# Kernel tuning notes

Hardware: AMD Instinct MI355X
Metric: run time of the kernel (lower is better)

Reference implementation:

```python
import jax, jax.numpy as jnp
import numpy as np

NUM_BEAMS = 2


def setup_inputs() -> dict:
    key = jax.random.key(0)
    ks = jax.random.split(key, 5)
    B, T, H, E, F = 128, 32, 768, 4, 3072
    x = jax.random.normal(ks[0], (B, T, H), dtype=jnp.float32)
    Wg = jax.random.normal(ks[1], (E, H), dtype=jnp.float32) * (1.0 / np.sqrt(H))
    W1 = jax.random.normal(ks[2], (E, H, F), dtype=jnp.float32) * (1.0 / np.sqrt(H))
    b1 = jnp.zeros((E, F), dtype=jnp.float32)
    W2 = jax.random.normal(ks[3], (E, F, H), dtype=jnp.float32) * (1.0 / np.sqrt(F))
    b2 = jnp.zeros((E, H), dtype=jnp.float32)
    return {"x": x, "Wg": Wg, "W1": W1, "b1": b1, "W2": W2, "b2": b2}


def reference(x, Wg, W1, b1, W2, b2):
    B, T, H = x.shape
    E = Wg.shape[0]
    nb = NUM_BEAMS
    # ---- forward_gate: mask is all-ones, so masked mean == mean over tokens ----
    x_avg = jnp.mean(x, axis=1)                          # [B, H]
    logits_gate = x_avg @ Wg.T                           # [B, E]
    prob_gate = jax.nn.softmax(logits_gate, axis=-1)     # [B, E]
    # ---- importance auxiliary loss (torch.std uses ddof=1) ----
    importance = jnp.sum(prob_gate, axis=0)              # [E]
    importance_loss = (jnp.std(importance, ddof=1) / jnp.mean(importance)) ** 2
    # ---- beam search, first layer: exp(log(p)) == p, top-k per row ----
    current_scores = jnp.exp(jnp.log(prob_gate))         # == prob_gate (kept for fidelity)
    topk_values, gate_idx = jax.lax.top_k(current_scores, nb)   # [B, nb]
    beam_scores = topk_values.reshape(nb * B)            # row-major flatten, matches .view
    expert_route = gate_idx.reshape(nb * B)[:, None]     # [B*nb, 1]
    beam_idx = jnp.arange(nb * B)
    current_expert_select = expert_route[:, -1]          # [B*nb]
    # ---- first layer: replicate x and scores along beam dim (interleaved) ----
    x_rep = jnp.repeat(x, nb, axis=0)                    # [B*nb, T, H]
    scores_rep = jnp.repeat(prob_gate, nb, axis=0)       # [B*nb, E]
    # input_x = x_rep[beam_idx] is identity here (beam_idx == arange)
    # ---- forward_expert_ffn: run ALL experts, mask+combine with gate prob ----
    h1 = jnp.einsum('bth,ehf->betf', x_rep, W1) + b1[None, :, None, :]
    h1 = jax.nn.gelu(h1, approximate=False)              # torch GELU is exact erf form
    cand = jnp.einsum('betf,efh->beth', h1, W2) + b2[None, :, None, :]  # [B*nb, E, T, H]
    weight = scores_rep * jax.nn.one_hot(current_expert_select, E, dtype=scores_rep.dtype)
    output = jnp.einsum('beth,be->bth', cand, weight)    # weighted sum over experts
    return output, beam_scores, expert_route, beam_idx, importance_loss
```

## Files before the change

### kernel.cpp

```cpp
#include <hip/hip_runtime.h>
#include <math.h>

typedef _Float16 f16;
typedef _Float16 f16x8 __attribute__((ext_vector_type(8)));
typedef float f32x4 __attribute__((ext_vector_type(4)));

#define Bn 128
#define Tn 32
#define Hn 768
#define En 4
#define Fn 3072
#define Rn 256
#define MAXT 67

static constexpr size_t OUT_ELEMS  = (size_t)Rn*Tn*Hn;
static constexpr size_t SCORES_OFF = OUT_ELEMS;
static constexpr size_t ROUTE_OFF  = OUT_ELEMS + Rn;
static constexpr size_t BIDX_OFF   = OUT_ELEMS + 2*Rn;
static constexpr size_t LOSS_OFF   = OUT_ELEMS + 3*Rn;

#define WS_WSF    0u
#define WS_ROUTE  4096u
#define WS_GRP    8192u
#define WS_X16    16384u
#define WS_W1T    (WS_X16 + 2u*Bn*Tn*Hn)
#define WS_W2T    (WS_W1T + 2u*En*Hn*Fn)
#define WS_H1     (WS_W2T + 2u*En*Fn*Hn)

#define GLOAD16(g, l) __builtin_amdgcn_global_load_lds( \
    (const __attribute__((address_space(1))) unsigned int*)(g), \
    (__attribute__((address_space(3))) unsigned int*)(l), 16, 0, 0)

__device__ __forceinline__ float fast_gelu(float v) {
  float s = v * 0.70710678118f;
  float a = fabsf(s);
  float t = 1.0f / (1.0f + 0.3275911f * a);
  float y = t*(0.254829592f + t*(-0.284496736f + t*(1.421413741f +
            t*(-1.453152027f + t*1.061405429f))));
  float er = 1.0f - y * __expf(-a*a);
  er = (s < 0.0f) ? -er : er;
  return 0.5f * v * (1.0f + er);
}

__global__ __launch_bounds__(64) void gate_kernel(
    const float* __restrict__ x, const float* __restrict__ Wg,
    float* __restrict__ out, float* __restrict__ wsf, int* __restrict__ route)
{
  const int b = blockIdx.x;
  const int l = threadIdx.x;
  float acc0=0.f, acc1=0.f, acc2=0.f, acc3=0.f;
  const float* xb = x + (size_t)b*Tn*Hn;
  for (int h = l; h < Hn; h += 64) {
    float xa = 0.f;
    #pragma unroll
    for (int t = 0; t < Tn; ++t) xa += xb[t*Hn + h];
    xa *= (1.0f/Tn);
    acc0 += xa * Wg[0*Hn + h];
    acc1 += xa * Wg[1*Hn + h];
    acc2 += xa * Wg[2*Hn + h];
    acc3 += xa * Wg[3*Hn + h];
  }
  #pragma unroll
  for (int o = 32; o > 0; o >>= 1) {
    acc0 += __shfl_down(acc0, o);
    acc1 += __shfl_down(acc1, o);
    acc2 += __shfl_down(acc2, o);
    acc3 += __shfl_down(acc3, o);
  }
  if (l == 0) {
    float lg[4] = {acc0, acc1, acc2, acc3};
    float m = fmaxf(fmaxf(lg[0],lg[1]), fmaxf(lg[2],lg[3]));
    float p[4]; float s = 0.f;
    #pragma unroll
    for (int e = 0; e < 4; ++e) { p[e] = expf(lg[e]-m); s += p[e]; }
    float inv = 1.f/s;
    #pragma unroll
    for (int e = 0; e < 4; ++e) { p[e] *= inv; wsf[b*4+e] = p[e]; }
    int i1 = 0;
    #pragma unroll
    for (int e = 1; e < 4; ++e) if (p[e] > p[i1]) i1 = e;
    int i2 = (i1 == 0) ? 1 : 0;
    #pragma unroll
    for (int e = 0; e < 4; ++e) if (e != i1 && p[e] > p[i2]) i2 = e;
    int idx[2] = {i1, i2};
    #pragma unroll
    for (int k = 0; k < 2; ++k) {
      int r = 2*b + k;
      float pv = p[idx[k]];
      wsf[512 + r] = pv;
      route[r] = idx[k];
      out[SCORES_OFF + r] = pv;
      out[ROUTE_OFF  + r] = (float)idx[k];
      out[BIDX_OFF   + r] = (float)r;
    }
  }
}

__global__ __launch_bounds__(64) void loss_kernel(
    const float* __restrict__ wsf, float* __restrict__ out)
{
  const int l = threadIdx.x;
  float i0=0.f,i1=0.f,i2=0.f,i3=0.f;
  for (int b = l; b < Bn; b += 64) {
    i0 += wsf[b*4+0]; i1 += wsf[b*4+1]; i2 += wsf[b*4+2]; i3 += wsf[b*4+3];
  }
  #pragma unroll
  for (int o = 32; o > 0; o >>= 1) {
    i0 += __shfl_down(i0,o); i1 += __shfl_down(i1,o);
    i2 += __shfl_down(i2,o); i3 += __shfl_down(i3,o);
  }
  if (l == 0) {
    float mean = 0.25f*(i0+i1+i2+i3);
    float d0=i0-mean, d1=i1-mean, d2=i2-mean, d3=i3-mean;
    float var = (d0*d0+d1*d1+d2*d2+d3*d3) * (1.f/3.f);
    out[LOSS_OFF] = var / (mean*mean);
  }
}

__global__ __launch_bounds__(64) void group_kernel(
    const int* __restrict__ route, int* __restrict__ grp)
{
  const int l = threadIdx.x;
  int cnt = 0;
  if (l < 4) { for (int r = 0; r < Rn; ++r) cnt += (route[r] == l); }
  int c0 = __shfl(cnt, 0), c1 = __shfl(cnt, 1), c2 = __shfl(cnt, 2), c3 = __shfl(cnt, 3);
  int off = (l >= 1 ? c0 : 0) + (l >= 2 ? c1 : 0) + (l >= 3 ? c2 : 0);
  if (l < 4) {
    int p = off;
    for (int r = 0; r < Rn; ++r) if (route[r] == l) grp[384 + p++] = r;
  }
  if (l == 0) {
    int cs[4] = {c0, c1, c2, c3};
    int os[4] = {0, c0, c0+c1, c0+c1+c2};
    int nt = 0;
    for (int e = 0; e < 4; ++e) {
      for (int s = 0; s < cs[e]; s += 4) {
        int nb = cs[e] - s; if (nb > 4) nb = 4;
        grp[8+nt*3+0] = e; grp[8+nt*3+1] = os[e]+s; grp[8+nt*3+2] = nb;
        ++nt;
      }
    }
    grp[0] = nt;
  }
}

__global__ __launch_bounds__(256) void convx_kernel(
    const float* __restrict__ x, f16* __restrict__ x16)
{
  const int i = (blockIdx.x*256 + threadIdx.x) * 8;
  float4 a = *(const float4*)(x + i);
  float4 b = *(const float4*)(x + i + 4);
  union { f16 h[8]; uint4 u; } p;
  p.h[0]=(f16)a.x; p.h[1]=(f16)a.y; p.h[2]=(f16)a.z; p.h[3]=(f16)a.w;
  p.h[4]=(f16)b.x; p.h[5]=(f16)b.y; p.h[6]=(f16)b.z; p.h[7]=(f16)b.w;
  *(uint4*)(x16 + i) = p.u;
}

__global__ __launch_bounds__(256) void transcvt_kernel(
    const float* __restrict__ src, f16* __restrict__ dst, int R, int C)
{
  __shared__ f16 t[64][74];
  const int e  = blockIdx.z;
  const int r0 = blockIdx.y*64, c0 = blockIdx.x*64;
  const float* s = src + (size_t)e*R*C;
  f16* d = dst + (size_t)e*R*C;
  const int tid = threadIdx.x;
  const int i  = tid >> 2;
  const int j0 = (tid & 3) * 16;
  #pragma unroll
  for (int q = 0; q < 16; q += 4) {
    float4 v = *(const float4*)(s + (size_t)(r0+i)*C + c0 + j0 + q);
    t[i][j0+q+0]=(f16)v.x; t[i][j0+q+1]=(f16)v.y; t[i][j0+q+2]=(f16)v.z; t[i][j0+q+3]=(f16)v.w;
  }
  __syncthreads();
  f16 o[16];
  #pragma unroll
  for (int q = 0; q < 16; ++q) o[q] = t[j0+q][i];
  *(uint4*)(d + (size_t)(c0+i)*R + r0 + j0)     = *(uint4*)&o[0];
  *(uint4*)(d + (size_t)(c0+i)*R + r0 + j0 + 8) = *(uint4*)&o[8];
}

template<int KD, int ND, int BN, int NWAVE, bool G1>
__global__ __launch_bounds__(NWAVE*64, 4) void gemm_kernel(
    const f16* __restrict__ A16, const f16* __restrict__ B16,
    const float* __restrict__ bias, f16* __restrict__ oh,
    float* __restrict__ of, const int* __restrict__ grp,
    const float* __restrict__ wsf)
{
  constexpr int NY  = ND / BN;
  constexpr int NWY = BN / 64;
  constexpr int BI_A = 128 / (NWAVE*16);
  constexpr int BI_B = BN  / (NWAVE*16);
  constexpr int NLD  = BI_A + BI_B;
  constexpr int BBUF = BN * 64;

  const int ntiles = grp[0];
  const int tix = blockIdx.x / NY;
  const int ny  = blockIdx.x % NY;
  if (tix >= ntiles) return;
  const int e      = grp[8+tix*3+0];
  const int bstart = grp[8+tix*3+1];
  const int nb     = grp[8+tix*3+2];
  const int n0     = ny * BN;
  const int tid    = threadIdx.x;
  const int lane   = tid & 63;
  const int w      = tid >> 6;

  extern __shared__ __align__(16) char smem[];

  const int srow  = lane >> 2;
  const int sunit = (lane & 3) ^ ((lane >> 3) & 3);
  const f16* asrc[BI_A];
  #pragma unroll
  for (int i = 0; i < BI_A; ++i) {
    int row = (w*BI_A + i)*16 + srow;
    int slot = row >> 5; if (slot >= nb) slot = nb - 1;
    int beam = grp[384 + bstart + slot];
    size_t rbase = G1 ? ((size_t)(beam>>1)*Tn + (row&31)) * (size_t)KD
                      : ((size_t)beam*Tn + (row&31)) * (size_t)KD;
    asrc[i] = A16 + rbase + sunit*8;
  }
  const f16* bsrc[BI_B];
  #pragma unroll
  for (int i = 0; i < BI_B; ++i) {
    int row = (w*BI_B + i)*16 + srow;
    bsrc[i] = B16 + (size_t)e*ND*KD + (size_t)(n0 + row)*KD + sunit*8;
  }

  const int wm = w / NWY, wn = w % NWY;
  const int lr = lane & 15, lk = lane >> 4;
  const int rowA0 = wm*64;
  const int rowB0 = wn*64;
  const int ub = (lk ^ ((lr >> 1) & 3)) << 4;

  f32x4 acc[4][4];
  #pragma unroll
  for (int i=0;i<4;++i)
    #pragma unroll
    for (int j=0;j<4;++j) acc[i][j] = (f32x4){0.f,0.f,0.f,0.f};

  constexpr int NT = KD/32;

  auto STAGE = [&](int bsel, int kt2) {
    char* Ad = smem + bsel*8192 + (w*BI_A)*1024;
    #pragma unroll
    for (int i = 0; i < BI_A; ++i) GLOAD16(asrc[i] + kt2*32, Ad + i*1024);
    char* Bd = smem + 16384 + bsel*BBUF + (w*BI_B)*1024;
    #pragma unroll
    for (int i = 0; i < BI_B; ++i) GLOAD16(bsrc[i] + kt2*32, Bd + i*1024);
  };

  STAGE(0, 0);

  int buf = 0;
  for (int kt = 0; kt < NT; ++kt) {
    if (kt + 1 < NT) {
      STAGE(buf ^ 1, kt + 1);
      asm volatile("s_waitcnt vmcnt(%0)" :: "i"(NLD) : "memory");
    } else {
      asm volatile("s_waitcnt vmcnt(0)" ::: "memory");
    }
    __builtin_amdgcn_sched_barrier(0);
    __builtin_amdgcn_s_barrier();
    __builtin_amdgcn_sched_barrier(0);

    const char* Ab = smem + buf*8192;
    const char* Bb = smem + 16384 + buf*BBUF;
    f16x8 af[4], bf[4];
    #pragma unroll
    for (int mi=0;mi<4;++mi)
      af[mi] = *(const f16x8*)(Ab + (rowA0 + mi*16 + lr)*64 + ub);
    #pragma unroll
    for (int ni=0;ni<4;++ni)
      bf[ni] = *(const f16x8*)(Bb + (rowB0 + ni*16 + lr)*64 + ub);
    __builtin_amdgcn_s_setprio(1);
    #pragma unroll
    for (int mi=0;mi<4;++mi)
      #pragma unroll
      for (int ni=0;ni<4;++ni)
        acc[mi][ni] = __builtin_amdgcn_mfma_f32_16x16x32_f16(af[mi], bf[ni], acc[mi][ni], 0, 0, 0);
    __builtin_amdgcn_s_setprio(0);
    __builtin_amdgcn_s_barrier();
    __builtin_amdgcn_sched_barrier(0);
    buf ^= 1;
  }

  const int nvalid = nb * Tn;
  char* cst = smem;
  float bvals[4];
  if (G1) {
    #pragma unroll
    for (int ni=0;ni<4;++ni) bvals[ni] = bias[e*ND + n0 + rowB0 + ni*16 + lr];
  }

  #pragma unroll
  for (int h = 0; h < 2; ++h) {
    if (wm == h) {
      #pragma unroll
      for (int mi=0;mi<4;++mi){
        #pragma unroll
        for (int j=0;j<4;++j){
          const int m = mi*16 + (lane>>4)*4 + j;
          const int m7 = m & 7;
          #pragma unroll
          for (int ni=0;ni<4;++ni){
            const int n = rowB0 + ni*16 + lr;
            if (G1) {
              float v = acc[mi][ni][j] + bvals[ni];
              *(f16*)(cst + m*512 + (((n>>3)^m7)<<4) + (n&7)*2) = (f16)fast_gelu(v);
            } else {
              *(float*)(cst + m*512 + (((n>>2)^m7)<<4) + (n&3)*4) = acc[mi][ni][j];
            }
          }
        }
      }
    }
    __syncthreads();
    const int u  = tid & 31;
    const int tr = tid >> 5;
    constexpr int RPI = NWAVE*2;
    #pragma unroll
    for (int it = 0; it < 64/RPI; ++it) {
      const int rl = it*RPI + tr;
      const int r  = h*64 + rl;
      if (r < nvalid) {
        const int beam = grp[384 + bstart + (r>>5)];
        if (G1) {
          uint4 v = *(const uint4*)(cst + rl*512 + (((u&24)|((u&7)^(rl&7)))<<4));
          *(uint4*)(oh + ((size_t)beam*Tn + (r&31))*(size_t)ND + n0 + u*8) = v;
        } else {
          float4 b4 = *(const float4*)(bias + e*ND + n0 + u*4);
          const float sc = wsf[512 + beam];
          float4 v = *(const float4*)(cst + rl*512 + (((u&24)|((u&7)^(rl&7)))<<4));
          v.x = (v.x + b4.x)*sc; v.y = (v.y + b4.y)*sc;
          v.z = (v.z + b4.z)*sc; v.w = (v.w + b4.w)*sc;
          *(float4*)(of + ((size_t)beam*Tn + (r&31))*(size_t)Hn + n0 + u*4) = v;
        }
      }
    }
    __syncthreads();
  }
}

extern "C" void kernel_launch(void* const* d_in, const int* in_sizes, int n_in,
                              void* d_out, int out_size, void* d_ws, size_t ws_size,
                              hipStream_t stream)
{
  const float* x  = (const float*)d_in[0];
  const float* Wg = (const float*)d_in[1];
  const float* W1 = (const float*)d_in[2];
  const float* b1 = (const float*)d_in[3];
  const float* W2 = (const float*)d_in[4];
  const float* b2 = (const float*)d_in[5];
  float* out = (float*)d_out;
  char* ws = (char*)d_ws;
  float* wsf  = (float*)(ws + WS_WSF);
  int*   route= (int*)(ws + WS_ROUTE);
  int*   grp  = (int*)(ws + WS_GRP);
  f16*   x16  = (f16*)(ws + WS_X16);
  f16*   w1t  = (f16*)(ws + WS_W1T);
  f16*   w2t  = (f16*)(ws + WS_W2T);
  f16*   h1   = (f16*)(ws + WS_H1);

  gate_kernel<<<Bn, 64, 0, stream>>>(x, Wg, out, wsf, route);
  group_kernel<<<1, 64, 0, stream>>>(route, grp);
  loss_kernel<<<1, 64, 0, stream>>>(wsf, out);
  convx_kernel<<<1536, 256, 0, stream>>>(x, x16);
  transcvt_kernel<<<dim3(48,12,4), 256, 0, stream>>>(W1, w1t, Hn, Fn);
  transcvt_kernel<<<dim3(12,48,4), 256, 0, stream>>>(W2, w2t, Fn, Hn);

  auto g1 = gemm_kernel<Hn, Fn, 256, 8, true>;
  auto g2 = gemm_kernel<Fn, Hn, 128, 4, false>;
  const int sm1 = 49152;
  const int sm2 = 32768;
  hipFuncSetAttribute((const void*)g1, hipFuncAttributeMaxDynamicSharedMemorySize, sm1);
  hipFuncSetAttribute((const void*)g2, hipFuncAttributeMaxDynamicSharedMemorySize, sm2);
  g1<<<MAXT*12, 512, sm1, stream>>>(x16, w1t, b1, h1, nullptr, grp, wsf);
  g2<<<MAXT*6,  256, sm2, stream>>>(h1, w2t, b2, nullptr, out, grp, wsf);
}
```

Before: 213.4 us.

## Triple-buffer GEMM k-loop with one barrier per step

Moves both GEMM kernels from double-buffered to triple-buffered shared memory, with A and B tiles interleaved in each buffer. Each k-step now issues a single barrier, then starts the load two steps ahead, then computes. This keeps more global loads in flight and removes the second barrier per iteration. Shared memory per block grows (to 72KB for the first GEMM), which may lower occupancy. The bias load in the second GEMM's epilogue is also hoisted out of the row loop.

```diff
diff --git a/kernel.cpp b/kernel.cpp
--- a/kernel.cpp
+++ b/kernel.cpp
@@ -192,7 +192,7 @@
   constexpr int BI_A = 128 / (NWAVE*16);
   constexpr int BI_B = BN  / (NWAVE*16);
   constexpr int NLD  = BI_A + BI_B;
-  constexpr int BBUF = BN * 64;
+  constexpr int BUFSZ = (128 + BN) * 64;
 
   const int ntiles = grp[0];
   const int tix = blockIdx.x / NY;
@@ -240,32 +240,20 @@
     for (int j=0;j<4;++j) acc[i][j] = (f32x4){0.f,0.f,0.f,0.f};
 
   constexpr int NT = KD/32;
+  static_assert(NT % 3 == 0, "NT must be divisible by 3");
 
   auto STAGE = [&](int bsel, int kt2) {
-    char* Ad = smem + bsel*8192 + (w*BI_A)*1024;
+    char* Ad = smem + bsel*BUFSZ + (w*BI_A)*1024;
     #pragma unroll
     for (int i = 0; i < BI_A; ++i) GLOAD16(asrc[i] + kt2*32, Ad + i*1024);
-    char* Bd = smem + 16384 + bsel*BBUF + (w*BI_B)*1024;
+    char* Bd = smem + bsel*BUFSZ + 8192 + (w*BI_B)*1024;
     #pragma unroll
     for (int i = 0; i < BI_B; ++i) GLOAD16(bsrc[i] + kt2*32, Bd + i*1024);
   };
 
-  STAGE(0, 0);
-
-  int buf = 0;
-  for (int kt = 0; kt < NT; ++kt) {
-    if (kt + 1 < NT) {
-      STAGE(buf ^ 1, kt + 1);
-      asm volatile("s_waitcnt vmcnt(%0)" :: "i"(NLD) : "memory");
-    } else {
-      asm volatile("s_waitcnt vmcnt(0)" ::: "memory");
-    }
-    __builtin_amdgcn_sched_barrier(0);
-    __builtin_amdgcn_s_barrier();
-    __builtin_amdgcn_sched_barrier(0);
-
-    const char* Ab = smem + buf*8192;
-    const char* Bb = smem + 16384 + buf*BBUF;
+  auto COMPUTE = [&](int b) {
+    const char* Ab = smem + b*BUFSZ;
+    const char* Bb = Ab + 8192;
     f16x8 af[4], bf[4];
     #pragma unroll
     for (int mi=0;mi<4;++mi)
@@ -280,10 +268,31 @@
       for (int ni=0;ni<4;++ni)
         acc[mi][ni] = __builtin_amdgcn_mfma_f32_16x16x32_f16(af[mi], bf[ni], acc[mi][ni], 0, 0, 0);
     __builtin_amdgcn_s_setprio(0);
-    __builtin_amdgcn_s_barrier();
-    __builtin_amdgcn_sched_barrier(0);
-    buf ^= 1;
-  }
+  };
+
+  STAGE(0, 0);
+  STAGE(1, 1);
+
+#define STEP(B, SB, KT2, VM, DOSTAGE) do { \
+    asm volatile("s_waitcnt vmcnt(%0)" :: "i"(VM) : "memory"); \
+    __builtin_amdgcn_sched_barrier(0); \
+    __builtin_amdgcn_s_barrier(); \
+    __builtin_amdgcn_sched_barrier(0); \
+    if (DOSTAGE) STAGE(SB, KT2); \
+    COMPUTE(B); \
+  } while (0)
+
+  for (int kt = 0; kt + 6 <= NT; kt += 3) {
+    STEP(0, 2, kt+2, NLD, true);
+    STEP(1, 0, kt+3, NLD, true);
+    STEP(2, 1, kt+4, NLD, true);
+  }
+  STEP(0, 2, NT-1, NLD, true);
+  STEP(1, 0, 0,    NLD, false);
+  STEP(2, 0, 0,    0,   false);
+#undef STEP
+
+  __builtin_amdgcn_s_barrier();
 
   const int nvalid = nb * Tn;
   char* cst = smem;
@@ -318,6 +327,8 @@
     __syncthreads();
     const int u  = tid & 31;
     const int tr = tid >> 5;
+    float4 b4;
+    if (!G1) b4 = *(const float4*)(bias + e*ND + n0 + u*4);
     constexpr int RPI = NWAVE*2;
     #pragma unroll
     for (int it = 0; it < 64/RPI; ++it) {
@@ -329,7 +340,6 @@
           uint4 v = *(const uint4*)(cst + rl*512 + (((u&24)|((u&7)^(rl&7)))<<4));
           *(uint4*)(oh + ((size_t)beam*Tn + (r&31))*(size_t)ND + n0 + u*8) = v;
         } else {
-          float4 b4 = *(const float4*)(bias + e*ND + n0 + u*4);
           const float sc = wsf[512 + beam];
           float4 v = *(const float4*)(cst + rl*512 + (((u&24)|((u&7)^(rl&7)))<<4));
           v.x = (v.x + b4.x)*sc; v.y = (v.y + b4.y)*sc;
@@ -371,8 +381,8 @@
 
   auto g1 = gemm_kernel<Hn, Fn, 256, 8, true>;
   auto g2 = gemm_kernel<Fn, Hn, 128, 4, false>;
-  const int sm1 = 49152;
-  const int sm2 = 32768;
+  const int sm1 = 3 * (128 + 256) * 64;
+  const int sm2 = 3 * (128 + 128) * 64;
   hipFuncSetAttribute((const void*)g1, hipFuncAttributeMaxDynamicSharedMemorySize, sm1);
   hipFuncSetAttribute((const void*)g2, hipFuncAttributeMaxDynamicSharedMemorySize, sm2);
   g1<<<MAXT*12, 512, sm1, stream>>>(x16, w1t, b1, h1, nullptr, grp, wsf);
```

Measured after the change: 212.9 us. Within noise of the previous version (-0.2%).
